# Optimization experiments

Hardware: AMD Instinct MI355X
Metric: run time of the kernel (lower is better)

Reference implementation:

```python
import jax, jax.numpy as jnp
import numpy as np

# ---------------- config (from ObjectDetector source) ----------------
B = 2; IMG = 224; STRIDE = 32; FH = IMG // STRIDE          # 7x7 feature map
C_FEAT = 1024
SIZES = (32., 64., 128., 256., 512.); RATIOS = (0.5, 1.0, 2.0)
A = len(SIZES) * len(RATIOS)                                # 15 anchors/loc
NA = FH * FH * A                                            # 735 anchors/img
PRE_NMS = min(1000, NA); POST_NMS = min(1000, NA)           # testing config
RPN_NMS_T = 0.7; RPN_MIN_SIZE = 1e-3
NUM_CLASSES = 37
ROI_OUT = 7; ROI_SR = 2; ROI_SCALE = 1.0 / STRIDE
REP = 1024
SCORE_T = 0.05; DET_NMS_T = 0.5; DETS_PER_IMG = 100
CAND_K = 2048            # candidate cap before final batched NMS
MIN_SIZE_DET = 1e-2
BBOX_CLIP = float(np.log(1000.0 / 16.0))


def make_anchors():
    scales = np.array(SIZES, np.float32); ratios = np.array(RATIOS, np.float32)
    h_r = np.sqrt(ratios); w_r = 1.0 / h_r
    ws = (w_r[:, None] * scales[None, :]).reshape(-1)
    hs = (h_r[:, None] * scales[None, :]).reshape(-1)
    base = np.round(np.stack([-ws, -hs, ws, hs], 1) / 2.0)   # [A,4]
    sy, sx = np.meshgrid(np.arange(FH) * STRIDE, np.arange(FH) * STRIDE, indexing='ij')
    shifts = np.stack([sx.reshape(-1), sy.reshape(-1), sx.reshape(-1), sy.reshape(-1)], 1).astype(np.float32)
    return jnp.asarray((shifts[:, None, :] + base[None, :, :]).reshape(-1, 4))  # [NA,4] (H,W,A)


def conv(x, w, b, stride=1, pad=0):
    y = jax.lax.conv_general_dilated(x, w, (stride, stride), [(pad, pad)] * 2,
                                     dimension_numbers=('NCHW', 'OIHW', 'NCHW'))
    return y + b[None, :, None, None]


def decode_boxes(deltas, boxes, weights):
    wx, wy, ww, wh = weights
    w = boxes[..., 2] - boxes[..., 0]; h = boxes[..., 3] - boxes[..., 1]
    cx = boxes[..., 0] + 0.5 * w; cy = boxes[..., 1] + 0.5 * h
    dx = deltas[..., 0] / wx; dy = deltas[..., 1] / wy
    dw = jnp.minimum(deltas[..., 2] / ww, BBOX_CLIP)
    dh = jnp.minimum(deltas[..., 3] / wh, BBOX_CLIP)
    pcx = dx * w + cx; pcy = dy * h + cy
    pw = jnp.exp(dw) * w; ph = jnp.exp(dh) * h
    return jnp.stack([pcx - 0.5 * pw, pcy - 0.5 * ph, pcx + 0.5 * pw, pcy + 0.5 * ph], -1)


def clip_boxes(b):
    x = jnp.clip(b[..., 0::2], 0.0, float(IMG)); y = jnp.clip(b[..., 1::2], 0.0, float(IMG))
    return jnp.stack([x[..., 0], y[..., 0], x[..., 1], y[..., 1]], -1)


def box_iou(a, b):
    area_a = (a[:, 2] - a[:, 0]) * (a[:, 3] - a[:, 1])
    area_b = (b[:, 2] - b[:, 0]) * (b[:, 3] - b[:, 1])
    lt = jnp.maximum(a[:, None, :2], b[None, :, :2])
    rb = jnp.minimum(a[:, None, 2:], b[None, :, 2:])
    wh = jnp.clip(rb - lt, 0.0, None)
    inter = wh[..., 0] * wh[..., 1]
    return inter / jnp.maximum(area_a[:, None] + area_b[None, :] - inter, 1e-9)


def nms_keep(boxes, scores, thresh):
    """Greedy NMS; returns keep mask in original order (fixed shapes)."""
    n = boxes.shape[0]
    order = jnp.argsort(-scores)
    iou = box_iou(*(jax.lax.stop_gradient(boxes[order]),) * 2)
    idx = jnp.arange(n)
    def body(i, keep):
        sup = (iou[i] > thresh) & (idx > i) & keep[i]
        return keep & ~sup
    keep_sorted = jax.lax.fori_loop(0, n, body, jnp.ones(n, bool))
    return jnp.zeros(n, bool).at[order].set(keep_sorted)


def rpn_filter_one(obj_logits, deltas, anchors):
    # obj_logits [NA], deltas [NA,4] (detached, as in torchvision RPN)
    top_v, top_i = jax.lax.top_k(obj_logits, PRE_NMS)
    boxes = clip_boxes(decode_boxes(deltas[top_i], anchors[top_i], (1., 1., 1., 1.)))
    prob = jax.nn.sigmoid(top_v)
    ws = boxes[:, 2] - boxes[:, 0]; hs = boxes[:, 3] - boxes[:, 1]
    prob = jnp.where((ws >= RPN_MIN_SIZE) & (hs >= RPN_MIN_SIZE), prob, -1.0)
    prob = jnp.where(nms_keep(boxes, prob, RPN_NMS_T), prob, -1.0)
    sv, si = jax.lax.top_k(prob, POST_NMS)
    return boxes[si], sv > 0.0


def bilinear(f_hwc, ys, xs):
    # torchvision roi_align bilinear sampling; f_hwc [H,W,C], ys/xs [R,O]
    H, W, _ = f_hwc.shape
    vy = (ys >= -1.0) & (ys <= H); vx = (xs >= -1.0) & (xs <= W)
    y = jnp.clip(ys, 0.0, None); x = jnp.clip(xs, 0.0, None)
    y0 = jnp.minimum(jnp.floor(y).astype(jnp.int32), H - 1)
    x0 = jnp.minimum(jnp.floor(x).astype(jnp.int32), W - 1)
    y1 = jnp.minimum(y0 + 1, H - 1); x1 = jnp.minimum(x0 + 1, W - 1)
    y = jnp.where(y0 == H - 1, y0.astype(y.dtype), y)
    x = jnp.where(x0 == W - 1, x0.astype(x.dtype), x)
    ly = y - y0; lx = x - x0; hy = 1.0 - ly; hx = 1.0 - lx
    g = lambda yi, xi: f_hwc[yi[:, :, None], xi[:, None, :]]   # [R,O,O,C]
    val = ((hy[:, :, None] * hx[:, None, :])[..., None] * g(y0, x0)
         + (hy[:, :, None] * lx[:, None, :])[..., None] * g(y0, x1)
         + (ly[:, :, None] * hx[:, None, :])[..., None] * g(y1, x0)
         + (ly[:, :, None] * lx[:, None, :])[..., None] * g(y1, x1))
    return val * (vy[:, :, None] & vx[:, None, :])[..., None]


def roi_align_one(feat_chw, rois):
    # feat [C,H,W], rois [R,4] -> [R,C,7,7]; output_size=7, sampling_ratio=2, scale=1/32
    f = jnp.transpose(feat_chw, (1, 2, 0))
    x1 = rois[:, 0] * ROI_SCALE; y1 = rois[:, 1] * ROI_SCALE
    rw = jnp.maximum(rois[:, 2] * ROI_SCALE - x1, 1.0)
    rh = jnp.maximum(rois[:, 3] * ROI_SCALE - y1, 1.0)
    bw = rw / ROI_OUT; bh = rh / ROI_OUT
    grid = jnp.arange(ROI_OUT, dtype=jnp.float32)
    acc = 0.0
    for iy in range(ROI_SR):
        ys = y1[:, None] + (grid[None, :] + (iy + 0.5) / ROI_SR) * bh[:, None]
        for ix in range(ROI_SR):
            xs = x1[:, None] + (grid[None, :] + (ix + 0.5) / ROI_SR) * bw[:, None]
            acc = acc + bilinear(f, ys, xs)
    return jnp.transpose(acc / (ROI_SR * ROI_SR), (0, 3, 1, 2))


def postprocess_one(logits, box_deltas, proposals, roi_valid):
    R = logits.shape[0]
    scores = jax.nn.softmax(logits, -1)
    boxes = clip_boxes(decode_boxes(box_deltas.reshape(R, NUM_CLASSES, 4),
                                    proposals[:, None, :], (10., 10., 5., 5.)))
    boxes = boxes[:, 1:, :].reshape(-1, 4)       # drop background class
    scores = jnp.where(roi_valid[:, None], scores[:, 1:], 0.0).reshape(-1)
    labels = jnp.broadcast_to(jnp.arange(1, NUM_CLASSES)[None, :], (R, NUM_CLASSES - 1)).reshape(-1)
    ws = boxes[:, 2] - boxes[:, 0]; hs = boxes[:, 3] - boxes[:, 1]
    ok = (ws >= MIN_SIZE_DET) & (hs >= MIN_SIZE_DET) & (scores > SCORE_T)
    cs, ci = jax.lax.top_k(jnp.where(ok, scores, -1.0), CAND_K)
    cb = boxes[ci]; cl = labels[ci]
    off = cl.astype(cb.dtype) * (IMG + 1.0)      # batched (per-class) NMS trick
    keep = nms_keep(cb + off[:, None], cs, DET_NMS_T)
    tv, ti = jax.lax.top_k(jnp.where(keep, cs, -1.0), DETS_PER_IMG)
    valid = tv > 0.0
    out_boxes = jnp.where(valid[:, None], cb[ti], 0.0)
    out_scores = jnp.where(valid, tv, 0.0)
    out_labels = jnp.where(valid, cl[ti], 0).astype(out_boxes.dtype)
    return jnp.concatenate([out_boxes, out_scores[:, None], out_labels[:, None]], -1)  # [100,6]


def forward(images, params, anchors):
    (bb_w, bb_b, rpn_w, rpn_b, cls_w, cls_b, reg_w, reg_b,
     fc1_w, fc1_b, fc2_w, fc2_b, clsp_w, clsp_b, boxp_w, boxp_b) = params
    Bn = images.shape[0]
    feats = jax.nn.relu(conv(images, bb_w, bb_b, stride=STRIDE))        # [B,1024,7,7]
    t = jax.nn.relu(conv(feats, rpn_w, rpn_b, stride=1, pad=1))
    obj = jnp.transpose(conv(t, cls_w, cls_b), (0, 2, 3, 1)).reshape(Bn, -1)            # [B,NA]
    reg = jnp.transpose(conv(t, reg_w, reg_b).reshape(Bn, A, 4, FH, FH),
                        (0, 3, 4, 1, 2)).reshape(Bn, -1, 4)                              # [B,NA,4]
    obj_d = jax.lax.stop_gradient(obj); reg_d = jax.lax.stop_gradient(reg)  # RPN detaches
    proposals, roi_valid = jax.vmap(lambda o, d: rpn_filter_one(o, d, anchors))(obj_d, reg_d)
    pooled = jax.vmap(roi_align_one)(feats, proposals)                  # [B,R,1024,7,7]
    x = pooled.reshape(Bn * POST_NMS, -1)
    x = jax.nn.relu(x @ fc1_w.T + fc1_b)
    x = jax.nn.relu(x @ fc2_w.T + fc2_b)
    logits = (x @ clsp_w.T + clsp_b).reshape(Bn, POST_NMS, NUM_CLASSES)
    bdelt = (x @ boxp_w.T + boxp_b).reshape(Bn, POST_NMS, NUM_CLASSES * 4)
    return jax.vmap(postprocess_one)(logits, bdelt, proposals, roi_valid)  # [B,100,6]


def setup_inputs() -> dict:
    key = jax.random.key(0)
    ks = jax.random.split(key, 10)
    w = lambda k, shape, s=0.02: jax.random.normal(k, shape, jnp.float32) * s
    return {
        'images': jax.random.uniform(ks[0], (B, 1, IMG, IMG), jnp.float32),
        'bb_w': w(ks[1], (C_FEAT, 1, STRIDE, STRIDE)), 'bb_b': jnp.zeros((C_FEAT,), jnp.float32),
        'rpn_w': w(ks[2], (C_FEAT, C_FEAT, 3, 3)), 'rpn_b': jnp.zeros((C_FEAT,), jnp.float32),
        'cls_w': w(ks[3], (A, C_FEAT, 1, 1)), 'cls_b': jnp.zeros((A,), jnp.float32),
        'reg_w': w(ks[4], (4 * A, C_FEAT, 1, 1)), 'reg_b': jnp.zeros((4 * A,), jnp.float32),
        'fc1_w': w(ks[5], (REP, C_FEAT * ROI_OUT * ROI_OUT), 0.005), 'fc1_b': jnp.zeros((REP,), jnp.float32),
        'fc2_w': w(ks[6], (REP, REP)), 'fc2_b': jnp.zeros((REP,), jnp.float32),
        'clsp_w': w(ks[7], (NUM_CLASSES, REP)), 'clsp_b': jnp.zeros((NUM_CLASSES,), jnp.float32),
        'boxp_w': w(ks[8], (NUM_CLASSES * 4, REP)), 'boxp_b': jnp.zeros((NUM_CLASSES * 4,), jnp.float32),
    }


def reference(images, bb_w, bb_b, rpn_w, rpn_b, cls_w, cls_b, reg_w, reg_b,
              fc1_w, fc1_b, fc2_w, fc2_b, clsp_w, clsp_b, boxp_w, boxp_b):
    anchors = make_anchors()
    params = (bb_w, bb_b, rpn_w, rpn_b, cls_w, cls_b, reg_w, reg_b,
              fc1_w, fc1_b, fc2_w, fc2_b, clsp_w, clsp_b, boxp_w, boxp_b)
    return forward(images, params, anchors)
```

## Files before the change

### kernel.cpp

```cpp
#include <hip/hip_runtime.h>
#include <math.h>

#define NANCH 735
#define NCAND 26460
#define NCANDP 26624
#define BBCLIP 4.135166556742356f
#define KF1 4864
#define KHALF 2432

typedef short bf16x8 __attribute__((ext_vector_type(8)));
typedef float f32x4 __attribute__((ext_vector_type(4)));

__device__ __forceinline__ unsigned short f2b(float f) {
  unsigned int u = __float_as_uint(f);
  unsigned int r = (u >> 16) & 1u;
  u += 0x7fffu + r;
  return (unsigned short)(u >> 16);
}

__device__ __forceinline__ void anchor_of(int i, float* o) {
  int pos = i / 15, a = i % 15;
  int iy = pos / 7, ix = pos % 7;
  int rr = a / 5, sc = a % 5;
  double ratio = (rr == 0) ? 0.5 : (rr == 1 ? 1.0 : 2.0);
  double scale = (double)(32 << sc);
  double hr = sqrt(ratio), wr = 1.0 / hr;
  double wsz = wr * scale, hsz = hr * scale;
  float bx1 = (float)rint(-wsz * 0.5), by1 = (float)rint(-hsz * 0.5);
  float bx2 = (float)rint(wsz * 0.5),  by2 = (float)rint(hsz * 0.5);
  float sx = (float)(ix * 32), sy = (float)(iy * 32);
  o[0] = sx + bx1; o[1] = sy + by1; o[2] = sx + bx2; o[3] = sy + by2;
}

__device__ __forceinline__ bool before_(float va, int ia, float vb, int ib) {
  return (va > vb) || (va == vb && ia < ib);
}

template<int NTOT, int NTH>
__device__ void bitonic_sort_sh(float* v, int* id) {
  const int t = threadIdx.x;
  for (int k = 2; k <= NTOT; k <<= 1) {
    for (int j = k >> 1; j > 0; j >>= 1) {
      for (int s = t; s < NTOT; s += NTH) {
        int p = s ^ j;
        if (p > s) {
          float v1 = v[s], v2 = v[p];
          int i1 = id[s], i2 = id[p];
          bool up = ((s & k) == 0);
          if (before_(v2, i2, v1, i1) == up) {
            v[s] = v2; id[s] = i2; v[p] = v1; id[p] = i1;
          }
        }
      }
      __syncthreads();
    }
  }
}

template<int NTOT, int NTH>
__device__ void bitonic_merge_sh(float* v, int* id) {
  const int t = threadIdx.x;
  for (int j = NTOT >> 1; j > 0; j >>= 1) {
    for (int s = t; s < NTOT; s += NTH) {
      int p = s ^ j;
      if (p > s) {
        float v1 = v[s], v2 = v[p];
        int i1 = id[s], i2 = id[p];
        if (before_(v2, i2, v1, i1)) {
          v[s] = v2; id[s] = i2; v[p] = v1; id[p] = i1;
        }
      }
    }
    __syncthreads();
  }
}

__global__ void k_im2col_bb(const float* __restrict__ images, unsigned short* __restrict__ patch) {
  int i = blockIdx.x * 256 + threadIdx.x;
  if (i >= 98 * 1024) return;
  int rowi = i >> 10, k = i & 1023;
  int b = rowi / 49, pos = rowi % 49;
  int oy = pos / 7, ox = pos % 7;
  int ky = k >> 5, kx = k & 31;
  patch[i] = f2b(images[((size_t)b * 224 + oy * 32 + ky) * 224 + ox * 32 + kx]);
}

__global__ void k_im2col_rpn(const unsigned short* __restrict__ bbh,
                             unsigned short* __restrict__ im2) {
  int i = blockIdx.x * 256 + threadIdx.x;
  if (i >= 98 * 9216) return;
  int rowi = i / 9216, k = i % 9216;
  int b = rowi / 49, pos = rowi % 49;
  int oy = pos / 7, ox = pos % 7;
  int ic = k / 9, kk = k % 9;
  int ky = kk / 3, kx = kk % 3;
  int y = oy + ky - 1, x = ox + kx - 1;
  unsigned short v = 0;
  if ((unsigned)y < 7u && (unsigned)x < 7u)
    v = bbh[((size_t)(b * 49 + y * 7 + x)) * 1024 + ic];
  im2[i] = v;
}

__global__ __launch_bounds__(256) void k_gemm_bf16(
    const unsigned short* __restrict__ A, int lda, int M,
    const unsigned short* __restrict__ B, int ldb,
    float* __restrict__ P, int N, int Kchunk,
    const int* __restrict__ nvalid)
// ... 49 lines not shown
      rB0 = *(const bf16x8*)(pB0 + ofs);
      rB1 = *(const bf16x8*)(pB1 + ofs);
    }
    bf16x8 af[4], bg[4];
#pragma unroll
    for (int i = 0; i < 4; ++i) af[i] = *(const bf16x8*)&As[cur][wm + i * 16 + fr][fk];
#pragma unroll
    for (int j = 0; j < 4; ++j) bg[j] = *(const bf16x8*)&Bs[cur][wn + j * 16 + fr][fk];
#pragma unroll
    for (int i = 0; i < 4; ++i)
#pragma unroll
      for (int j = 0; j < 4; ++j)
        acc[i][j] = __builtin_amdgcn_mfma_f32_16x16x32_bf16(af[i], bg[j], acc[i][j], 0, 0, 0);
    cur ^= 1;
  }
  float* Pp = P + (size_t)bz * M * N;
#pragma unroll
  for (int i = 0; i < 4; ++i) {
#pragma unroll
    for (int r = 0; r < 4; ++r) {
      int gm = m0 + wm + i * 16 + (lane >> 4) * 4 + r;
      if (gm < M) {
#pragma unroll
        for (int j = 0; j < 4; ++j)
          Pp[(size_t)gm * N + n0 + wn + j * 16 + (lane & 15)] = acc[i][j][r];
      }
    }
  }
}

__global__ __launch_bounds__(256) void k_gemm_mb(
    const unsigned short* __restrict__ A,
    const unsigned short* __restrict__ W1p,
    float* __restrict__ Mb)
{
  __shared__ __attribute__((aligned(16))) unsigned short As[2][128][40];
  __shared__ __attribute__((aligned(16))) unsigned short Bs[2][128][40];
  const int G = gridDim.x * gridDim.y * gridDim.z;
  int lid = blockIdx.x + gridDim.x * (blockIdx.y + gridDim.y * blockIdx.z);
  lid = (lid & 7) * (G >> 3) + (lid >> 3);
  const int rest = lid;
  const int by = rest % gridDim.y, p = rest / gridDim.y;
  const int n0 = by * 128;
  const int M = 98;
  const unsigned short* B = W1p + (size_t)p * 1048576;
  const int t = threadIdx.x;
  const int lane = t & 63, wid = t >> 6;
  const int wm = (wid >> 1) * 64, wn = (wid & 1) * 64;
  f32x4 acc[4][4];
#pragma unroll
  for (int i = 0; i < 4; ++i)
#pragma unroll
    for (int j = 0; j < 4; ++j) acc[i][j] = (f32x4){0.f, 0.f, 0.f, 0.f};
  const int r0 = t >> 2, c0 = (t & 3) * 8;
  const int fr = lane & 15, fk = (lane >> 4) * 8;
  int gA0 = r0; if (gA0 >= M) gA0 = M - 1;
  int gA1 = r0 + 64; if (gA1 >= M) gA1 = M - 1;
  const unsigned short* pA0 = A + (size_t)gA0 * 1024 + c0;
  const unsigned short* pA1 = A + (size_t)gA1 * 1024 + c0;
  const unsigned short* pB0 = B + (size_t)(n0 + r0) * 1024 + c0;
  const unsigned short* pB1 = B + (size_t)(n0 + r0 + 64) * 1024 + c0;
  bf16x8 rA0 = *(const bf16x8*)pA0;
  bf16x8 rA1 = *(const bf16x8*)pA1;
  bf16x8 rB0 = *(const bf16x8*)pB0;
  bf16x8 rB1 = *(const bf16x8*)pB1;
  const int nt = 1024 >> 5;
  int cur = 0;
  for (int it = 0; it < nt; ++it) {
    *(bf16x8*)&As[cur][r0][c0] = rA0;
    *(bf16x8*)&As[cur][r0 + 64][c0] = rA1;
    *(bf16x8*)&Bs[cur][r0][c0] = rB0;
    *(bf16x8*)&Bs[cur][r0 + 64][c0] = rB1;
    __syncthreads();
    if (it + 1 < nt) {
      size_t ofs = (size_t)(it + 1) * 32;
      rA0 = *(const bf16x8*)(pA0 + ofs);
      rA1 = *(const bf16x8*)(pA1 + ofs);
      rB0 = *(const bf16x8*)(pB0 + ofs);
      rB1 = *(const bf16x8*)(pB1 + ofs);
    }
    bf16x8 af[4], bg[4];
#pragma unroll
    for (int i = 0; i < 4; ++i) af[i] = *(const bf16x8*)&As[cur][wm + i * 16 + fr][fk];
#pragma unroll
    for (int j = 0; j < 4; ++j) bg[j] = *(const bf16x8*)&Bs[cur][wn + j * 16 + fr][fk];
#pragma unroll
    for (int i = 0; i < 4; ++i)
#pragma unroll
      for (int j = 0; j < 4; ++j)
        acc[i][j] = __builtin_amdgcn_mfma_f32_16x16x32_bf16(af[i], bg[j], acc[i][j], 0, 0, 0);
    cur ^= 1;
  }
  float* Pp = Mb + (size_t)p * 98 * 1024;
#pragma unroll
  for (int i = 0; i < 4; ++i) {
#pragma unroll
    for (int r = 0; r < 4; ++r) {
      int gm = wm + i * 16 + (lane >> 4) * 4 + r;
      if (gm < M) {
#pragma unroll
        for (int j = 0; j < 4; ++j)
          Pp[(size_t)gm * 1024 + n0 + wn + j * 16 + (lane & 15)] = acc[i][j][r];
      }
    }
  }
}

__global__ __launch_bounds__(256) void k_mtrans(const float* __restrict__ Mb,
                                                unsigned short* __restrict__ Bmat)
{
  __shared__ float tile[98][129];
  const int p = blockIdx.x, n0 = blockIdx.y * 128;
  const int t = threadIdx.x;
  for (int j = t; j < 98 * 128; j += 256) {
    int q = j >> 7, nl = j & 127;
    tile[q][nl] = Mb[((size_t)p * 98 + q) * 1024 + n0 + nl];
  }
  __syncthreads();
  for (int j = t; j < 128 * 98; j += 256) {
    int nl = j / 98, q2 = j % 98;
    int bb = q2 >= 49 ? 1 : 0;
    int col = bb * KHALF + p * 49 + (q2 - bb * 49);
    Bmat[(size_t)(n0 + nl) * KF1 + col] = f2b(tile[q2][nl]);
  }
  if (p == 0) {
    for (int j = t; j < 128 * 62; j += 256) {
      int nl = j / 62, e = j % 62;
      int bb = e >= 31 ? 1 : 0;
      int col = bb * KHALF + 2401 + (e - bb * 31);
      Bmat[(size_t)(n0 + nl) * KF1 + col] = 0;
    }
  }
}

__global__ __launch_bounds__(256) void k_gbuild(const float* __restrict__ props,
                                                unsigned short* __restrict__ Gmat)
{
#pragma clang fp contract(off)
  int rg = blockIdx.x;
  int b = rg / NANCH;
  __shared__ float g[KF1];
  int t = threadIdx.x;
  for (int j = t; j < KF1; j += 256) g[j] = 0.f;
  __syncthreads();
  if (t < 49) {
    const float* roi = props + (size_t)rg * 4;
    int p = t, oy = p / 7, ox = p % 7;
    float x1 = roi[0] * 0.03125f, y1 = roi[1] * 0.03125f;
    float rw = fmaxf(roi[2] * 0.03125f - x1, 1.f);
    float rh = fmaxf(roi[3] * 0.03125f - y1, 1.f);
    float bw = rw / 7.f, bh = rh / 7.f;
    float* gb = g + b * KHALF + p * 49;
    for (int iy = 0; iy < 2; ++iy) {
      for (int ix = 0; ix < 2; ++ix) {
        float ys = y1 + ((float)oy + ((float)iy + 0.5f) * 0.5f) * bh;
        float xs = x1 + ((float)ox + ((float)ix + 0.5f) * 0.5f) * bw;
// ... 62 lines not shown
    tile[cl * 50 + p] = f2b(src[i]);
  }
  __syncthreads();
  for (int j = t; j < 6272; j += 256) {
    int p = j >> 7, cl = j & 127;
    o[((size_t)p * 1024 + n) * 1024 + (size_t)ct * 128 + cl] = tile[cl * 50 + p];
  }
}

__global__ __launch_bounds__(256) void k_rpn_head(
    const float* __restrict__ tmn, const float* __restrict__ cls_w,
    const float* __restrict__ cls_b, const float* __restrict__ reg_w,
    const float* __restrict__ reg_b, float* __restrict__ obj, float* __restrict__ reg)
{
  int blk = blockIdx.x;
  __shared__ float col[1024];
  const float* row = tmn + (size_t)blk * 1024;
  for (int i = threadIdx.x; i < 1024; i += 256) col[i] = row[i];
  __syncthreads();
  int b = blk / 49, pos = blk % 49;
  for (int o = threadIdx.x; o < 75; o += 256) {
    const float* w = (o < 15) ? (cls_w + (size_t)o * 1024) : (reg_w + (size_t)(o - 15) * 1024);
    float s = 0.f;
    for (int k = 0; k < 1024; ++k) s = fmaf(col[k], w[k], s);
    if (o < 15) {
      obj[(size_t)b * NANCH + pos * 15 + o] = s + cls_b[o];
    } else {
      int c = o - 15, a = c >> 2, d = c & 3;
      reg[((size_t)b * NANCH + pos * 15 + a) * 4 + d] = s + reg_b[c];
    }
  }
}

__global__ __launch_bounds__(1024) void k_rpn_prep(
    const float* __restrict__ obj, const float* __restrict__ reg,
    float* __restrict__ bxp, float* __restrict__ pnms)
{
#pragma clang fp contract(off)
  const int b = blockIdx.x, t = threadIdx.x;
  __shared__ float sval[1024];
  __shared__ float vo1[1024];
  __shared__ int o1a[1024];
  __shared__ int wtv[16];
  __shared__ int wti[16];
  sval[t] = (t < NANCH) ? obj[(size_t)b * NANCH + t] : -INFINITY;
  __syncthreads();
  {
    float v = sval[t];
    int rank = 0;
    for (int j = 0; j < NANCH; ++j) {
      float u = sval[j];
      rank += (u > v) || (u == v && j < t);
    }
    if (t < NANCH) { vo1[rank] = v; o1a[rank] = t; }
  }
  __syncthreads();
  float x1 = 0.f, y1 = 0.f, x2 = 0.f, y2 = 0.f, prob = -1.f;
  bool flag = false;
  if (t < NANCH) {
    int ai = o1a[t];
    const float* d = reg + ((size_t)b * NANCH + ai) * 4;
    float an[4];
    anchor_of(ai, an);
    float aw = an[2] - an[0], ah = an[3] - an[1];
    float acx = an[0] + 0.5f * aw, acy = an[1] + 0.5f * ah;
    float dw = fminf(d[2], BBCLIP), dh = fminf(d[3], BBCLIP);
    float pcx = d[0] * aw + acx, pcy = d[1] * ah + acy;
    float pw = expf(dw) * aw, ph = expf(dh) * ah;
    x1 = pcx - 0.5f * pw; y1 = pcy - 0.5f * ph;
    x2 = pcx + 0.5f * pw; y2 = pcy + 0.5f * ph;
    x1 = fminf(fmaxf(x1, 0.f), 224.f);
    y1 = fminf(fmaxf(y1, 0.f), 224.f);
    x2 = fminf(fmaxf(x2, 0.f), 224.f);
    y2 = fminf(fmaxf(y2, 0.f), 224.f);
    flag = (x2 - x1 >= 1e-3f) && (y2 - y1 >= 1e-3f);
    prob = 1.f / (1.f + expf(-vo1[t]));
  }
  bool iflag = (t < NANCH) && !flag;
  unsigned long long balv = __ballot(flag);
  unsigned long long bali = __ballot(iflag);
  int lane = t & 63, w = t >> 6;
  if (lane == 0) { wtv[w] = __popcll(balv); wti[w] = __popcll(bali); }
  __syncthreads();
  int nval = 0, basev = 0, basei = 0;
  for (int k = 0; k < 16; ++k) {
    int cv = wtv[k], ci = wti[k];
    nval += cv;
    if (k < w) { basev += cv; basei += ci; }
  }
  if (t < NANCH) {
    unsigned long long lm = (1ull << lane) - 1;
    int pos = flag ? (basev + __popcll(balv & lm))
                   : (nval + basei + __popcll(bali & lm));
    float* o = bxp + ((size_t)b * NANCH + pos) * 4;
    o[0] = x1; o[1] = y1; o[2] = x2; o[3] = y2;
    pnms[(size_t)b * NANCH + pos] = flag ? prob : -1.f;
  }
}

__global__ __launch_bounds__(256) void k_rpn_mask(
    const float* __restrict__ bxp, unsigned long long* __restrict__ rmask)
{
#pragma clang fp contract(off)
  int blk = blockIdx.x;
  int b = blk / 35;
  int row = (blk % 35) * 21 + (int)(threadIdx.x / 12);
  int w = threadIdx.x % 12;
  if (threadIdx.x >= 252 || row >= NANCH) return;
  const float* a = bxp + ((size_t)b * NANCH + row) * 4;
  float a0 = a[0], a1 = a[1], a2 = a[2], a3 = a[3];
  float aarea = (a2 - a0) * (a3 - a1);
  int l0 = w * 64;
  int l1 = (l0 + 64 < NANCH) ? l0 + 64 : NANCH;
  int ls = (l0 > row + 1) ? l0 : row + 1;
  unsigned long long bits = 0ull;
  for (int l = ls; l < l1; ++l) {
    const float* q = bxp + ((size_t)b * NANCH + l) * 4;
    float b0 = q[0], b1 = q[1], b2 = q[2], b3 = q[3];
    float barea = (b2 - b0) * (b3 - b1);
    float ix1 = fmaxf(a0, b0), iy1 = fmaxf(a1, b1);
    float ix2 = fminf(a2, b2), iy2 = fminf(a3, b3);
    float iw = fmaxf(ix2 - ix1, 0.f), ih = fmaxf(iy2 - iy1, 0.f);
    float inter = iw * ih;
    float iou = inter / fmaxf(aarea + barea - inter, 1e-9f);
    if (iou > 0.7f) bits |= 1ull << (l & 63);
  }
  rmask[((size_t)b * NANCH + row) * 12 + w] = bits;
}

__global__ __launch_bounds__(1024) void k_rpn_fin(
    const float* __restrict__ bxp, const float* __restrict__ pnms,
    const unsigned long long* __restrict__ rmask,
    float* __restrict__ props, int* __restrict__ meta)
{
  const int b = blockIdx.x, t = threadIdx.x;
  __shared__ unsigned long long smask[NANCH * 12];
  __shared__ float sp[1024];
  __shared__ unsigned long long keepw[12];
  __shared__ int wtot[16];
  for (int i = t; i < NANCH * 12; i += 1024)
    smask[i] = rmask[(size_t)b * NANCH * 12 + i];
  sp[t] = (t < NANCH) ? pnms[(size_t)b * NANCH + t] : -1.f;
  __syncthreads();
  if (t < 64) {
    unsigned long long kl = (t < 12) ? ~0ull : 0ull;
    for (int i = 0; i < NANCH; ++i) {
      unsigned long long kw = __shfl(kl, i >> 6);
      unsigned long long m = (t < 12) ? smask[i * 12 + t] : 0ull;
      bool on = (kw >> (i & 63)) & 1ull;
      kl &= on ? ~m : ~0ull;
    }
    if (t < 12) keepw[t] = kl;
  }
  __syncthreads();
  bool flag = false;
  if (t < NANCH) {
    bool kp = (keepw[t >> 6] >> (t & 63)) & 1ull;
    flag = kp && (sp[t] > 0.f);
  }
  unsigned long long bal = __ballot(flag);
  int lane = t & 63, w = t >> 6;
  if (lane == 0) wtot[w] = __popcll(bal);
  __syncthreads();
  int base = 0, tot = 0;
  for (int k = 0; k < 16; ++k) { int c = wtot[k]; if (k < w) base += c; tot += c; }
  if (flag) {
    int pos = base + __popcll(bal & ((1ull << lane) - 1));
    const float* src = bxp + ((size_t)b * NANCH + t) * 4;
    float* o = props + ((size_t)b * NANCH + pos) * 4;
    o[0] = src[0]; o[1] = src[1]; o[2] = src[2]; o[3] = src[3];
  }
  if (t == 0) meta[b] = tot;
}

__global__ __launch_bounds__(256) void k_heads(
    const float* __restrict__ h2, const float* __restrict__ cw,
    const float* __restrict__ cb, const float* __restrict__ bw_,
    const float* __restrict__ bb_, const int* __restrict__ meta,
    float* __restrict__ logits, float* __restrict__ bdelt)
{
  int rg = blockIdx.x;
  int b = rg / NANCH, r = rg % NANCH;
  if (r >= meta[b]) return;
  __shared__ float row[1024];
  for (int i = threadIdx.x; i < 1024; i += 256) row[i] = h2[(size_t)rg * 1024 + i];
  __syncthreads();
  for (int o = threadIdx.x; o < 185; o += 256) {
    const float* w = (o < 37) ? (cw + (size_t)o * 1024) : (bw_ + (size_t)(o - 37) * 1024);
    float s = 0.f;
    for (int k = 0; k < 1024; ++k) s = fmaf(row[k], w[k], s);
    if (o < 37) logits[(size_t)rg * 37 + o] = s + cb[o];
    else bdelt[(size_t)rg * 148 + (o - 37)] = s + bb_[o - 37];
  }
}

__global__ void k_cand(const float* __restrict__ logits, const float* __restrict__ bdelt,
                       const float* __restrict__ props, const int* __restrict__ meta,
                       float* __restrict__ cscore, float* __restrict__ cbox)
{
#pragma clang fp contract(off)
  int rg = blockIdx.x * blockDim.x + threadIdx.x;
  if (rg >= 2 * NANCH) return;
  int b = rg / NANCH, r = rg % NANCH;
  float* cs = cscore + (size_t)b * NCANDP;
  float* cb = cbox + (size_t)b * NCANDP * 4;
  int base = r * 36;
  if (r >= meta[b]) {
    for (int j = 0; j < 36; ++j) {
      cs[base + j] = -1.f;
      float* q = cb + (size_t)(base + j) * 4;
      q[0] = 0.f; q[1] = 0.f; q[2] = 0.f; q[3] = 0.f;
    }
    return;
  }
  const float* lg = logits + (size_t)rg * 37;
  float mx = lg[0];
  for (int c = 1; c < 37; ++c) mx = fmaxf(mx, lg[c]);
  float sum = 0.f;
  for (int c = 0; c < 37; ++c) sum += expf(lg[c] - mx);
  const float* roi = props + (size_t)rg * 4;
  float rw = roi[2] - roi[0], rh = roi[3] - roi[1];
  float rcx = roi[0] + 0.5f * rw, rcy = roi[1] + 0.5f * rh;
  const float* dd = bdelt + (size_t)rg * 148;
  for (int c = 1; c < 37; ++c) {
    const float* d = dd + c * 4;
    float dx = d[0] / 10.f, dy = d[1] / 10.f;
    float dw = fminf(d[2] / 5.f, BBCLIP), dh = fminf(d[3] / 5.f, BBCLIP);
    float pcx = dx * rw + rcx, pcy = dy * rh + rcy;
    float pw = expf(dw) * rw, ph = expf(dh) * rh;
    float x1 = pcx - 0.5f * pw, y1 = pcy - 0.5f * ph;
    float x2 = pcx + 0.5f * pw, y2 = pcy + 0.5f * ph;
    x1 = fminf(fmaxf(x1, 0.f), 224.f);
    y1 = fminf(fmaxf(y1, 0.f), 224.f);
    x2 = fminf(fmaxf(x2, 0.f), 224.f);
    y2 = fminf(fmaxf(y2, 0.f), 224.f);
    float sc = expf(lg[c] - mx) / sum;
    bool ok = ((x2 - x1) >= 1e-2f) && ((y2 - y1) >= 1e-2f) && (sc > 0.05f);
    cs[base + c - 1] = ok ? sc : -1.f;
    float* q = cb + (size_t)(base + c - 1) * 4;
    q[0] = x1; q[1] = y1; q[2] = x2; q[3] = y2;
  }
}

__global__ __launch_bounds__(1024) void k_top2048(
    const float* __restrict__ cscore,
    float* __restrict__ sel_score, int* __restrict__ sel_cidx,
    int* __restrict__ meta)
{
  const int b = blockIdx.x, t = threadIdx.x;
  __shared__ float Lv[2048]; __shared__ int Li[2048];
  __shared__ float Cv[2048]; __shared__ int Ci[2048];
  __shared__ int cnt;
  const float* cs = cscore + (size_t)b * NCANDP;
  if (t == 0) cnt = 0;
  __syncthreads();
  for (int gi = t; gi < NCAND; gi += 1024) {
    float v = cs[gi];
    if (v > 0.f) {
      int p = atomicAdd(&cnt, 1);
      if (p < 2048) { Cv[p] = v; Ci[p] = gi; }
    }
  }
  __syncthreads();
  int npos = cnt;
  if (npos <= 2048) {
    for (int h = 0; h < 2; ++h) {
      int p = h * 1024 + t;
      if (p < npos) {
        float v = Cv[p]; int id = Ci[p];
        int rank = 0;
        for (int j = 0; j < npos; ++j) {
          float u = Cv[j]; int ju = Ci[j];
          rank += (u > v) || (u == v && ju < id);
// ... 157 lines not shown
  (void)in_sizes; (void)n_in; (void)out_size; (void)ws_size;
  const float* images = (const float*)d_in[0];
  const float* bb_w   = (const float*)d_in[1];
  const float* bb_b   = (const float*)d_in[2];
  const float* rpn_w  = (const float*)d_in[3];
  const float* rpn_b  = (const float*)d_in[4];
  const float* cls_w  = (const float*)d_in[5];
  const float* cls_b  = (const float*)d_in[6];
  const float* reg_w  = (const float*)d_in[7];
  const float* reg_b  = (const float*)d_in[8];
  const float* fc1_w  = (const float*)d_in[9];
  const float* fc1_b  = (const float*)d_in[10];
  const float* fc2_w  = (const float*)d_in[11];
  const float* fc2_b  = (const float*)d_in[12];
  const float* clsp_w = (const float*)d_in[13];
  const float* clsp_b = (const float*)d_in[14];
  const float* boxp_w = (const float*)d_in[15];
  const float* boxp_b = (const float*)d_in[16];
  float* out = (float*)d_out;
  char* ws = (char*)d_ws;

  size_t off = 0;
  auto alloc = [&](size_t bytes) -> size_t {
    size_t o = off; off = (off + bytes + 255) & ~(size_t)255; return o;
  };
  size_t o_patch = alloc(98ull * 1024 * 2);
  size_t o_bbC   = alloc(98ull * 1024 * 4);
  size_t o_bbh   = alloc(98ull * 1024 * 2);
  size_t o_t     = alloc(98ull * 1024 * 4);
  size_t o_im2   = alloc(98ull * 9216 * 2);
  size_t o_obj   = alloc(1470ull * 4);
  size_t o_reg   = alloc(1470ull * 16);
  size_t o_props = alloc(1470ull * 16);
  size_t o_bxp   = alloc(1470ull * 16);
  size_t o_pnms  = alloc(1470ull * 4);
  size_t o_rm    = alloc(1470ull * 12 * 8);
  size_t o_meta  = alloc(256);
  size_t o_y1    = alloc(1470ull * 1024 * 4);
  size_t o_y2    = alloc(1470ull * 1024 * 4);
  size_t o_log   = alloc(1470ull * 37 * 4);
  size_t o_bd    = alloc(1470ull * 148 * 4);
  size_t o_cs    = alloc(2ull * NCANDP * 4);
  size_t o_cb    = alloc(2ull * NCANDP * 16);
  size_t o_ss    = alloc(2ull * 2048 * 4);
  size_t o_sc    = alloc(2ull * 2048 * 4);
  size_t o_dm    = alloc(2ull * 2048 * 32 * 8);
  size_t o_w0b   = alloc(1048576ull * 2);
  size_t o_w3b   = alloc(9437184ull * 2);
  size_t o_w1p   = alloc(51380224ull * 2);
  size_t o_mbuf  = alloc(49ull * 98 * 1024 * 4);
  size_t o_bmat  = alloc(1024ull * KF1 * 2);
  size_t o_gmat  = alloc(1470ull * KF1 * 2);
  size_t o_w2b   = alloc(1048576ull * 2);
  size_t o_y1b   = alloc(1470ull * 1024 * 2);
  size_t o_P     = alloc(32ull * 98 * 1024 * 4 > 4ull * 1470 * 1024 * 4
                         ? 32ull * 98 * 1024 * 4 : 4ull * 1470 * 1024 * 4);

  unsigned short* patchb = (unsigned short*)(ws + o_patch);
  float* bbC   = (float*)(ws + o_bbC);
  unsigned short* bbh = (unsigned short*)(ws + o_bbh);
  float* tb    = (float*)(ws + o_t);
  unsigned short* im2b = (unsigned short*)(ws + o_im2);
  float* objb  = (float*)(ws + o_obj);
  float* regb  = (float*)(ws + o_reg);
  float* props = (float*)(ws + o_props);
  float* bxp   = (float*)(ws + o_bxp);
  float* pnms  = (float*)(ws + o_pnms);
  unsigned long long* rmb = (unsigned long long*)(ws + o_rm);
  int*   meta  = (int*)(ws + o_meta);
  float* y1    = (float*)(ws + o_y1);
  float* y2    = (float*)(ws + o_y2);
  float* logb  = (float*)(ws + o_log);
  float* bdb   = (float*)(ws + o_bd);
  float* csb   = (float*)(ws + o_cs);
  float* cbb   = (float*)(ws + o_cb);
  float* ssb   = (float*)(ws + o_ss);
  int*   scb   = (int*)(ws + o_sc);
  unsigned long long* dmb = (unsigned long long*)(ws + o_dm);
  unsigned short* w0b = (unsigned short*)(ws + o_w0b);
  unsigned short* w3b = (unsigned short*)(ws + o_w3b);
  unsigned short* w1p = (unsigned short*)(ws + o_w1p);
  float* mbuf  = (float*)(ws + o_mbuf);
  unsigned short* bmat = (unsigned short*)(ws + o_bmat);
  unsigned short* gmat = (unsigned short*)(ws + o_gmat);
  unsigned short* w2b = (unsigned short*)(ws + o_w2b);
  unsigned short* y1b = (unsigned short*)(ws + o_y1b);
  float* Pb    = (float*)(ws + o_P);

  k_w1perm2<<<dim3(1024, 8), 256, 0, stream>>>(fc1_w, w1p);
  k_f2b3<<<11264, 256, 0, stream>>>(fc2_w, w2b, bb_w, w0b, rpn_w, w3b);
  k_im2col_bb<<<392, 256, 0, stream>>>(images, patchb);
  k_gemm_bf16<<<dim3(1, 8, 8), 256, 0, stream>>>(patchb, 1024, 98, w0b, 1024, Pb, 1024, 128, nullptr);
  k_reduce<<<392, 256, 0, stream>>>(Pb, bbC, bbh, 8, 98, 1024, bb_b, 31);
  k_gemm_mb<<<dim3(1, 8, 49), 256, 0, stream>>>(bbh, w1p, mbuf);
  k_mtrans<<<dim3(49, 8), 256, 0, stream>>>(mbuf, bmat);
  k_im2col_rpn<<<3528, 256, 0, stream>>>(bbh, im2b);
  k_gemm_bf16<<<dim3(1, 8, 32), 256, 0, stream>>>(im2b, 9216, 98, w3b, 9216, Pb, 1024, 288, nullptr);
  k_reduce<<<392, 256, 0, stream>>>(Pb, tb, nullptr, 32, 98, 1024, rpn_b, 7);
  k_rpn_head<<<98, 256, 0, stream>>>(tb, cls_w, cls_b, reg_w, reg_b, objb, regb);
  k_rpn_prep<<<2, 1024, 0, stream>>>(objb, regb, bxp, pnms);
  k_rpn_mask<<<70, 256, 0, stream>>>(bxp, rmb);
  k_rpn_fin<<<2, 1024, 0, stream>>>(bxp, pnms, rmb, props, meta);
  k_gbuild<<<1470, 256, 0, stream>>>(props, gmat);
  k_gemm_bf16<<<dim3(12, 8, 4), 256, 0, stream>>>(gmat, KF1, 1470, bmat, KF1, Pb, 1024, 1216, meta);
  k_reduce<<<5880, 256, 0, stream>>>(Pb, y1, y1b, 4, 1470, 1024, fc1_b, 31);
  k_gemm_bf16<<<dim3(12, 8, 2), 256, 0, stream>>>(y1b, 1024, 1470, w2b, 1024, Pb, 1024, 512, meta);
  k_reduce<<<5880, 256, 0, stream>>>(Pb, y2, nullptr, 2, 1470, 1024, fc2_b, 7);
  k_heads<<<1470, 256, 0, stream>>>(y2, clsp_w, clsp_b, boxp_w, boxp_b, meta, logb, bdb);
  k_cand<<<6, 256, 0, stream>>>(logb, bdb, props, meta, csb, cbb);
  k_top2048<<<2, 1024, 0, stream>>>(csb, ssb, scb, meta);
  k_detmask<<<512, 256, 0, stream>>>(scb, cbb, meta, dmb);
  k_final<<<2, 1024, 0, stream>>>(ssb, scb, cbb, dmb, meta, out);
}
```

Measured before the change: 498.0 us.

## Fuse RPN NMS kernels and detection heads with candidate generation

```diff
diff --git a/kernel.cpp b/kernel.cpp
--- a/kernel.cpp
+++ b/kernel.cpp
@@ -30,49 +30,6 @@
   float bx2 = (float)rint(wsz * 0.5),  by2 = (float)rint(hsz * 0.5);
   float sx = (float)(ix * 32), sy = (float)(iy * 32);
   o[0] = sx + bx1; o[1] = sy + by1; o[2] = sx + bx2; o[3] = sy + by2;
-}
-
-__device__ __forceinline__ bool before_(float va, int ia, float vb, int ib) {
-  return (va > vb) || (va == vb && ia < ib);
-}
-
-template<int NTOT, int NTH>
-__device__ void bitonic_sort_sh(float* v, int* id) {
-  const int t = threadIdx.x;
-  for (int k = 2; k <= NTOT; k <<= 1) {
-    for (int j = k >> 1; j > 0; j >>= 1) {
-      for (int s = t; s < NTOT; s += NTH) {
-        int p = s ^ j;
-        if (p > s) {
-          float v1 = v[s], v2 = v[p];
-          int i1 = id[s], i2 = id[p];
-          bool up = ((s & k) == 0);
-          if (before_(v2, i2, v1, i1) == up) {
-            v[s] = v2; id[s] = i2; v[p] = v1; id[p] = i1;
-          }
-        }
-      }
-      __syncthreads();
-    }
-  }
-}
-
-template<int NTOT, int NTH>
-__device__ void bitonic_merge_sh(float* v, int* id) {
-  const int t = threadIdx.x;
-  for (int j = NTOT >> 1; j > 0; j >>= 1) {
-    for (int s = t; s < NTOT; s += NTH) {
-      int p = s ^ j;
-      if (p > s) {
-        float v1 = v[s], v2 = v[p];
-        int i1 = id[s], i2 = id[p];
-        if (before_(v2, i2, v1, i1)) {
-          v[s] = v2; id[s] = i2; v[p] = v1; id[p] = i1;
-        }
-      }
-    }
-    __syncthreads();
-  }
 }
 
 __global__ void k_im2col_bb(const float* __restrict__ images, unsigned short* __restrict__ patch) {
@@ -188,7 +145,7 @@
 __global__ __launch_bounds__(256) void k_gemm_mb(
     const unsigned short* __restrict__ A,
     const unsigned short* __restrict__ W1p,
-    float* __restrict__ Mb)
+    unsigned short* __restrict__ Mbh)
 {
   __shared__ __attribute__((aligned(16))) unsigned short As[2][128][40];
   __shared__ __attribute__((aligned(16))) unsigned short Bs[2][128][40];
@@ -247,7 +204,7 @@
         acc[i][j] = __builtin_amdgcn_mfma_f32_16x16x32_bf16(af[i], bg[j], acc[i][j], 0, 0, 0);
     cur ^= 1;
   }
-  float* Pp = Mb + (size_t)p * 98 * 1024;
+  unsigned short* Pp = Mbh + (size_t)p * 98 * 1024;
 #pragma unroll
   for (int i = 0; i < 4; ++i) {
 #pragma unroll
@@ -256,28 +213,28 @@
       if (gm < M) {
 #pragma unroll
         for (int j = 0; j < 4; ++j)
-          Pp[(size_t)gm * 1024 + n0 + wn + j * 16 + (lane & 15)] = acc[i][j][r];
+          Pp[(size_t)gm * 1024 + n0 + wn + j * 16 + (lane & 15)] = f2b(acc[i][j][r]);
       }
     }
   }
 }
 
-__global__ __launch_bounds__(256) void k_mtrans(const float* __restrict__ Mb,
+__global__ __launch_bounds__(256) void k_mtrans(const unsigned short* __restrict__ Mbh,
                                                 unsigned short* __restrict__ Bmat)
 {
-  __shared__ float tile[98][129];
+  __shared__ unsigned short tile[98][129];
   const int p = blockIdx.x, n0 = blockIdx.y * 128;
   const int t = threadIdx.x;
   for (int j = t; j < 98 * 128; j += 256) {
     int q = j >> 7, nl = j & 127;
-    tile[q][nl] = Mb[((size_t)p * 98 + q) * 1024 + n0 + nl];
+    tile[q][nl] = Mbh[((size_t)p * 98 + q) * 1024 + n0 + nl];
   }
   __syncthreads();
   for (int j = t; j < 128 * 98; j += 256) {
     int nl = j / 98, q2 = j % 98;
     int bb = q2 >= 49 ? 1 : 0;
     int col = bb * KHALF + p * 49 + (q2 - bb * 49);
-    Bmat[(size_t)(n0 + nl) * KF1 + col] = f2b(tile[q2][nl]);
+    Bmat[(size_t)(n0 + nl) * KF1 + col] = tile[q2][nl];
   }
   if (p == 0) {
     for (int j = t; j < 128 * 62; j += 256) {
@@ -406,9 +363,9 @@
   }
 }
 
-__global__ __launch_bounds__(1024) void k_rpn_prep(
+__global__ __launch_bounds__(1024) void k_rpn_all(
     const float* __restrict__ obj, const float* __restrict__ reg,
-    float* __restrict__ bxp, float* __restrict__ pnms)
+    float* __restrict__ props, int* __restrict__ meta)
 {
 #pragma clang fp contract(off)
   const int b = blockIdx.x, t = threadIdx.x;
@@ -417,6 +374,12 @@
   __shared__ int o1a[1024];
   __shared__ int wtv[16];
   __shared__ int wti[16];
+  __shared__ float bx4[736][4];
+  __shared__ float pb[736];
+  __shared__ unsigned long long smask[NANCH * 12];
+  __shared__ unsigned long long keepw[12];
+  __shared__ int wtot[16];
+
   sval[t] = (t < NANCH) ? obj[(size_t)b * NANCH + t] : -INFINITY;
   __syncthreads();
   {
@@ -466,55 +429,32 @@
     unsigned long long lm = (1ull << lane) - 1;
     int pos = flag ? (basev + __popcll(balv & lm))
                    : (nval + basei + __popcll(bali & lm));
-    float* o = bxp + ((size_t)b * NANCH + pos) * 4;
-    o[0] = x1; o[1] = y1; o[2] = x2; o[3] = y2;
-    pnms[(size_t)b * NANCH + pos] = flag ? prob : -1.f;
-  }
-}
-
-__global__ __launch_bounds__(256) void k_rpn_mask(
-    const float* __restrict__ bxp, unsigned long long* __restrict__ rmask)
-{
-#pragma clang fp contract(off)
-  int blk = blockIdx.x;
-  int b = blk / 35;
-  int row = (blk % 35) * 21 + (int)(threadIdx.x / 12);
-  int w = threadIdx.x % 12;
-  if (threadIdx.x >= 252 || row >= NANCH) return;
-  const float* a = bxp + ((size_t)b * NANCH + row) * 4;
-  float a0 = a[0], a1 = a[1], a2 = a[2], a3 = a[3];
-  float aarea = (a2 - a0) * (a3 - a1);
-  int l0 = w * 64;
-  int l1 = (l0 + 64 < NANCH) ? l0 + 64 : NANCH;
-  int ls = (l0 > row + 1) ? l0 : row + 1;
-  unsigned long long bits = 0ull;
-  for (int l = ls; l < l1; ++l) {
-    const float* q = bxp + ((size_t)b * NANCH + l) * 4;
-    float b0 = q[0], b1 = q[1], b2 = q[2], b3 = q[3];
-    float barea = (b2 - b0) * (b3 - b1);
-    float ix1 = fmaxf(a0, b0), iy1 = fmaxf(a1, b1);
-    float ix2 = fminf(a2, b2), iy2 = fminf(a3, b3);
-    float iw = fmaxf(ix2 - ix1, 0.f), ih = fmaxf(iy2 - iy1, 0.f);
-    float inter = iw * ih;
-    float iou = inter / fmaxf(aarea + barea - inter, 1e-9f);
-    if (iou > 0.7f) bits |= 1ull << (l & 63);
-  }
-  rmask[((size_t)b * NANCH + row) * 12 + w] = bits;
-}
-
-__global__ __launch_bounds__(1024) void k_rpn_fin(
-    const float* __restrict__ bxp, const float* __restrict__ pnms,
-    const unsigned long long* __restrict__ rmask,
-    float* __restrict__ props, int* __restrict__ meta)
-{
-  const int b = blockIdx.x, t = threadIdx.x;
-  __shared__ unsigned long long smask[NANCH * 12];
-  __shared__ float sp[1024];
-  __shared__ unsigned long long keepw[12];
-  __shared__ int wtot[16];
-  for (int i = t; i < NANCH * 12; i += 1024)
-    smask[i] = rmask[(size_t)b * NANCH * 12 + i];
-  sp[t] = (t < NANCH) ? pnms[(size_t)b * NANCH + t] : -1.f;
+    bx4[pos][0] = x1; bx4[pos][1] = y1; bx4[pos][2] = x2; bx4[pos][3] = y2;
+    pb[pos] = flag ? prob : -1.f;
+  }
+  __syncthreads();
+  for (int wk = t; wk < NANCH * 12; wk += 1024) {
+    int row = wk / 12, wd = wk % 12;
+    unsigned long long bits = 0ull;
+    const float* a = bx4[row];
+    float a0 = a[0], a1 = a[1], a2 = a[2], a3 = a[3];
+    float aarea = (a2 - a0) * (a3 - a1);
+    int l0 = wd * 64;
+    int l1 = (l0 + 64 < NANCH) ? l0 + 64 : NANCH;
+    int ls = (l0 > row + 1) ? l0 : row + 1;
+    for (int l = ls; l < l1; ++l) {
+      const float* q = bx4[l];
+      float b0 = q[0], b1 = q[1], b2 = q[2], b3 = q[3];
+      float barea = (b2 - b0) * (b3 - b1);
+      float ix1 = fmaxf(a0, b0), iy1 = fmaxf(a1, b1);
+      float ix2 = fminf(a2, b2), iy2 = fminf(a3, b3);
+      float iw = fmaxf(ix2 - ix1, 0.f), ih = fmaxf(iy2 - iy1, 0.f);
+      float inter = iw * ih;
+      float iou = inter / fmaxf(aarea + barea - inter, 1e-9f);
+      if (iou > 0.7f) bits |= 1ull << (l & 63);
+    }
+    smask[row * 12 + wd] = bits;
+  }
   __syncthreads();
   if (t < 64) {
     unsigned long long kl = (t < 12) ? ~0ull : 0ull;
@@ -527,77 +467,74 @@
     if (t < 12) keepw[t] = kl;
   }
   __syncthreads();
-  bool flag = false;
+  bool kflag = false;
   if (t < NANCH) {
     bool kp = (keepw[t >> 6] >> (t & 63)) & 1ull;
-    flag = kp && (sp[t] > 0.f);
-  }
-  unsigned long long bal = __ballot(flag);
-  int lane = t & 63, w = t >> 6;
+    kflag = kp && (pb[t] > 0.f);
+  }
+  unsigned long long bal = __ballot(kflag);
   if (lane == 0) wtot[w] = __popcll(bal);
   __syncthreads();
   int base = 0, tot = 0;
   for (int k = 0; k < 16; ++k) { int c = wtot[k]; if (k < w) base += c; tot += c; }
-  if (flag) {
+  if (kflag) {
     int pos = base + __popcll(bal & ((1ull << lane) - 1));
-    const float* src = bxp + ((size_t)b * NANCH + t) * 4;
     float* o = props + ((size_t)b * NANCH + pos) * 4;
-    o[0] = src[0]; o[1] = src[1]; o[2] = src[2]; o[3] = src[3];
+    o[0] = bx4[t][0]; o[1] = bx4[t][1]; o[2] = bx4[t][2]; o[3] = bx4[t][3];
   }
   if (t == 0) meta[b] = tot;
 }
 
-__global__ __launch_bounds__(256) void k_heads(
+__global__ __launch_bounds__(256) void k_headcand(
     const float* __restrict__ h2, const float* __restrict__ cw,
     const float* __restrict__ cb, const float* __restrict__ bw_,
     const float* __restrict__ bb_, const int* __restrict__ meta,
-    float* __restrict__ logits, float* __restrict__ bdelt)
-{
+    const float* __restrict__ props,
+    float* __restrict__ cscore, float* __restrict__ cbox)
+{
+#pragma clang fp contract(off)
   int rg = blockIdx.x;
   int b = rg / NANCH, r = rg % NANCH;
-  if (r >= meta[b]) return;
+  float* cs = cscore + (size_t)b * NCANDP;
+  float* cbx = cbox + (size_t)b * NCANDP * 4;
+  int base = r * 36;
+  if (r >= meta[b]) {
+    int j = threadIdx.x;
+    if (j < 36) {
+      cs[base + j] = -1.f;
+      float* q = cbx + (size_t)(base + j) * 4;
+      q[0] = 0.f; q[1] = 0.f; q[2] = 0.f; q[3] = 0.f;
+    }
+    return;
+  }
   __shared__ float row[1024];
+  __shared__ float lg[37];
+  __shared__ float bd[148];
+  __shared__ float mxsum[2];
   for (int i = threadIdx.x; i < 1024; i += 256) row[i] = h2[(size_t)rg * 1024 + i];
   __syncthreads();
   for (int o = threadIdx.x; o < 185; o += 256) {
     const float* w = (o < 37) ? (cw + (size_t)o * 1024) : (bw_ + (size_t)(o - 37) * 1024);
     float s = 0.f;
     for (int k = 0; k < 1024; ++k) s = fmaf(row[k], w[k], s);
-    if (o < 37) logits[(size_t)rg * 37 + o] = s + cb[o];
-    else bdelt[(size_t)rg * 148 + (o - 37)] = s + bb_[o - 37];
-  }
-}
-
-__global__ void k_cand(const float* __restrict__ logits, const float* __restrict__ bdelt,
-                       const float* __restrict__ props, const int* __restrict__ meta,
-                       float* __restrict__ cscore, float* __restrict__ cbox)
-{
-#pragma clang fp contract(off)
-  int rg = blockIdx.x * blockDim.x + threadIdx.x;
-  if (rg >= 2 * NANCH) return;
-  int b = rg / NANCH, r = rg % NANCH;
-  float* cs = cscore + (size_t)b * NCANDP;
-  float* cb = cbox + (size_t)b * NCANDP * 4;
-  int base = r * 36;
-  if (r >= meta[b]) {
-    for (int j = 0; j < 36; ++j) {
-      cs[base + j] = -1.f;
-      float* q = cb + (size_t)(base + j) * 4;
-      q[0] = 0.f; q[1] = 0.f; q[2] = 0.f; q[3] = 0.f;
-    }
-    return;
-  }
-  const float* lg = logits + (size_t)rg * 37;
-  float mx = lg[0];
-  for (int c = 1; c < 37; ++c) mx = fmaxf(mx, lg[c]);
-  float sum = 0.f;
-  for (int c = 0; c < 37; ++c) sum += expf(lg[c] - mx);
-  const float* roi = props + (size_t)rg * 4;
-  float rw = roi[2] - roi[0], rh = roi[3] - roi[1];
-  float rcx = roi[0] + 0.5f * rw, rcy = roi[1] + 0.5f * rh;
-  const float* dd = bdelt + (size_t)rg * 148;
-  for (int c = 1; c < 37; ++c) {
-    const float* d = dd + c * 4;
+    if (o < 37) lg[o] = s + cb[o];
+    else bd[o - 37] = s + bb_[o - 37];
+  }
+  __syncthreads();
+  if (threadIdx.x == 0) {
+    float mx = lg[0];
+    for (int c = 1; c < 37; ++c) mx = fmaxf(mx, lg[c]);
+    float sum = 0.f;
+    for (int c = 0; c < 37; ++c) sum += expf(lg[c] - mx);
+    mxsum[0] = mx; mxsum[1] = sum;
+  }
+  __syncthreads();
+  int c = threadIdx.x + 1;
+  if (c <= 36) {
+    const float* roi = props + (size_t)rg * 4;
+    float rw = roi[2] - roi[0], rh = roi[3] - roi[1];
+    float rcx = roi[0] + 0.5f * rw, rcy = roi[1] + 0.5f * rh;
+    const float* d = bd + c * 4;
     float dx = d[0] / 10.f, dy = d[1] / 10.f;
     float dw = fminf(d[2] / 5.f, BBCLIP), dh = fminf(d[3] / 5.f, BBCLIP);
     float pcx = dx * rw + rcx, pcy = dy * rh + rcy;
@@ -608,11 +545,54 @@
     y1 = fminf(fmaxf(y1, 0.f), 224.f);
     x2 = fminf(fmaxf(x2, 0.f), 224.f);
     y2 = fminf(fmaxf(y2, 0.f), 224.f);
-    float sc = expf(lg[c] - mx) / sum;
+    float sc = expf(lg[c] - mxsum[0]) / mxsum[1];
     bool ok = ((x2 - x1) >= 1e-2f) && ((y2 - y1) >= 1e-2f) && (sc > 0.05f);
     cs[base + c - 1] = ok ? sc : -1.f;
-    float* q = cb + (size_t)(base + c - 1) * 4;
+    float* q = cbx + (size_t)(base + c - 1) * 4;
     q[0] = x1; q[1] = y1; q[2] = x2; q[3] = y2;
+  }
+}
+
+__device__ __forceinline__ bool before_(float va, int ia, float vb, int ib) {
+  return (va > vb) || (va == vb && ia < ib);
+}
+
+template<int NTOT, int NTH>
+__device__ void bitonic_sort_sh(float* v, int* id) {
+  const int t = threadIdx.x;
+  for (int k = 2; k <= NTOT; k <<= 1) {
+    for (int j = k >> 1; j > 0; j >>= 1) {
+      for (int s = t; s < NTOT; s += NTH) {
+        int p = s ^ j;
+        if (p > s) {
+          float v1 = v[s], v2 = v[p];
+          int i1 = id[s], i2 = id[p];
+          bool up = ((s & k) == 0);
+          if (before_(v2, i2, v1, i1) == up) {
+            v[s] = v2; id[s] = i2; v[p] = v1; id[p] = i1;
+          }
+        }
+      }
+      __syncthreads();
+    }
+  }
+}
+
+template<int NTOT, int NTH>
+__device__ void bitonic_merge_sh(float* v, int* id) {
+  const int t = threadIdx.x;
+  for (int j = NTOT >> 1; j > 0; j >>= 1) {
+    for (int s = t; s < NTOT; s += NTH) {
+      int p = s ^ j;
+      if (p > s) {
+        float v1 = v[s], v2 = v[p];
+        int i1 = id[s], i2 = id[p];
+        if (before_(v2, i2, v1, i1)) {
+          v[s] = v2; id[s] = i2; v[p] = v1; id[p] = i1;
+        }
+      }
+    }
+    __syncthreads();
   }
 }
 
@@ -836,14 +816,9 @@
   size_t o_obj   = alloc(1470ull * 4);
   size_t o_reg   = alloc(1470ull * 16);
   size_t o_props = alloc(1470ull * 16);
-  size_t o_bxp   = alloc(1470ull * 16);
-  size_t o_pnms  = alloc(1470ull * 4);
-  size_t o_rm    = alloc(1470ull * 12 * 8);
   size_t o_meta  = alloc(256);
   size_t o_y1    = alloc(1470ull * 1024 * 4);
   size_t o_y2    = alloc(1470ull * 1024 * 4);
-  size_t o_log   = alloc(1470ull * 37 * 4);
-  size_t o_bd    = alloc(1470ull * 148 * 4);
   size_t o_cs    = alloc(2ull * NCANDP * 4);
   size_t o_cb    = alloc(2ull * NCANDP * 16);
   size_t o_ss    = alloc(2ull * 2048 * 4);
@@ -852,7 +827,7 @@
   size_t o_w0b   = alloc(1048576ull * 2);
   size_t o_w3b   = alloc(9437184ull * 2);
   size_t o_w1p   = alloc(51380224ull * 2);
-  size_t o_mbuf  = alloc(49ull * 98 * 1024 * 4);
+  size_t o_mbh   = alloc(49ull * 98 * 1024 * 2);
   size_t o_bmat  = alloc(1024ull * KF1 * 2);
   size_t o_gmat  = alloc(1470ull * KF1 * 2);
   size_t o_w2b   = alloc(1048576ull * 2);
@@ -868,14 +843,9 @@
   float* objb  = (float*)(ws + o_obj);
   float* regb  = (float*)(ws + o_reg);
   float* props = (float*)(ws + o_props);
-  float* bxp   = (float*)(ws + o_bxp);
-  float* pnms  = (float*)(ws + o_pnms);
-  unsigned long long* rmb = (unsigned long long*)(ws + o_rm);
   int*   meta  = (int*)(ws + o_meta);
   float* y1    = (float*)(ws + o_y1);
   float* y2    = (float*)(ws + o_y2);
-  float* logb  = (float*)(ws + o_log);
-  float* bdb   = (float*)(ws + o_bd);
   float* csb   = (float*)(ws + o_cs);
   float* cbb   = (float*)(ws + o_cb);
   float* ssb   = (float*)(ws + o_ss);
@@ -884,7 +854,7 @@
   unsigned short* w0b = (unsigned short*)(ws + o_w0b);
   unsigned short* w3b = (unsigned short*)(ws + o_w3b);
   unsigned short* w1p = (unsigned short*)(ws + o_w1p);
-  float* mbuf  = (float*)(ws + o_mbuf);
+  unsigned short* mbh = (unsigned short*)(ws + o_mbh);
   unsigned short* bmat = (unsigned short*)(ws + o_bmat);
   unsigned short* gmat = (unsigned short*)(ws + o_gmat);
   unsigned short* w2b = (unsigned short*)(ws + o_w2b);
@@ -896,22 +866,19 @@
   k_im2col_bb<<<392, 256, 0, stream>>>(images, patchb);
   k_gemm_bf16<<<dim3(1, 8, 8), 256, 0, stream>>>(patchb, 1024, 98, w0b, 1024, Pb, 1024, 128, nullptr);
   k_reduce<<<392, 256, 0, stream>>>(Pb, bbC, bbh, 8, 98, 1024, bb_b, 31);
-  k_gemm_mb<<<dim3(1, 8, 49), 256, 0, stream>>>(bbh, w1p, mbuf);
-  k_mtrans<<<dim3(49, 8), 256, 0, stream>>>(mbuf, bmat);
+  k_gemm_mb<<<dim3(1, 8, 49), 256, 0, stream>>>(bbh, w1p, mbh);
+  k_mtrans<<<dim3(49, 8), 256, 0, stream>>>(mbh, bmat);
   k_im2col_rpn<<<3528, 256, 0, stream>>>(bbh, im2b);
   k_gemm_bf16<<<dim3(1, 8, 32), 256, 0, stream>>>(im2b, 9216, 98, w3b, 9216, Pb, 1024, 288, nullptr);
   k_reduce<<<392, 256, 0, stream>>>(Pb, tb, nullptr, 32, 98, 1024, rpn_b, 7);
   k_rpn_head<<<98, 256, 0, stream>>>(tb, cls_w, cls_b, reg_w, reg_b, objb, regb);
-  k_rpn_prep<<<2, 1024, 0, stream>>>(objb, regb, bxp, pnms);
-  k_rpn_mask<<<70, 256, 0, stream>>>(bxp, rmb);
-  k_rpn_fin<<<2, 1024, 0, stream>>>(bxp, pnms, rmb, props, meta);
+  k_rpn_all<<<2, 1024, 0, stream>>>(objb, regb, props, meta);
   k_gbuild<<<1470, 256, 0, stream>>>(props, gmat);
   k_gemm_bf16<<<dim3(12, 8, 4), 256, 0, stream>>>(gmat, KF1, 1470, bmat, KF1, Pb, 1024, 1216, meta);
   k_reduce<<<5880, 256, 0, stream>>>(Pb, y1, y1b, 4, 1470, 1024, fc1_b, 31);
   k_gemm_bf16<<<dim3(12, 8, 2), 256, 0, stream>>>(y1b, 1024, 1470, w2b, 1024, Pb, 1024, 512, meta);
   k_reduce<<<5880, 256, 0, stream>>>(Pb, y2, nullptr, 2, 1470, 1024, fc2_b, 7);
-  k_heads<<<1470, 256, 0, stream>>>(y2, clsp_w, clsp_b, boxp_w, boxp_b, meta, logb, bdb);
-  k_cand<<<6, 256, 0, stream>>>(logb, bdb, props, meta, csb, cbb);
+  k_headcand<<<1470, 256, 0, stream>>>(y2, clsp_w, clsp_b, boxp_w, boxp_b, meta, props, csb, cbb);
   k_top2048<<<2, 1024, 0, stream>>>(csb, ssb, scb, meta);
   k_detmask<<<512, 256, 0, stream>>>(scb, cbb, meta, dmb);
   k_final<<<2, 1024, 0, stream>>>(ssb, scb, cbb, dmb, meta, out);
```

Result: slower. 566.4 us (+13.7%).
